# Kernel optimization log

Hardware: AMD Instinct MI355X
Metric: run time of the kernel (lower is better)

The kernel has to match this reference:

```python
import jax, jax.numpy as jnp
import numpy as np

B, H, W, C = 32, 56, 56, 192
WS, SHIFT, HEADS = 7, 3, 6
HEAD_DIM = C // HEADS
SCALE = 0.17677669529663687  # 1/sqrt(32), passed as qk_scale
HIDDEN = 4 * C
N = WS * WS
EPS = 1e-3


def _rel_index(ws):
    coords = np.stack(np.meshgrid(np.arange(ws), np.arange(ws), indexing='ij')).reshape(2, -1)
    rel = (coords[:, :, None] - coords[:, None, :]).transpose(1, 2, 0)
    rel[:, :, 0] += ws - 1
    rel[:, :, 1] += ws - 1
    rel[:, :, 0] *= 2 * ws - 1
    return rel.sum(-1)  # [N, N] int


def _attn_mask(h, w, ws, ss):
    img = np.zeros((h, w), np.float32)
    cnt = 0
    for hs in (slice(0, -ws), slice(-ws, -ss), slice(-ss, None)):
        for wsl in (slice(0, -ws), slice(-ws, -ss), slice(-ss, None)):
            img[hs, wsl] = cnt
            cnt += 1
    win = img.reshape(h // ws, ws, w // ws, ws).transpose(0, 2, 1, 3).reshape(-1, ws * ws)
    diff = win[:, None, :] - win[:, :, None]
    return np.where(diff != 0, -100.0, 0.0).astype(np.float32)  # [nW, N, N]


REL_IDX = jnp.asarray(_rel_index(WS).reshape(-1))          # [N*N]
ATTN_MASK = jnp.asarray(_attn_mask(H, W, WS, SHIFT))       # [nW, N, N]
NW = ATTN_MASK.shape[0]


def _window_partition(x, ws):
    b, h, w, c = x.shape
    x = x.reshape(b, h // ws, ws, w // ws, ws, c).transpose(0, 1, 3, 2, 4, 5)
    return x.reshape(-1, ws, ws, c)


def _window_reverse(x, ws, h, w):
    c = x.shape[-1]
    x = x.reshape(-1, h // ws, w // ws, ws, ws, c).transpose(0, 1, 3, 2, 4, 5)
    return x.reshape(-1, h, w, c)


def _layer_norm(x, g, b):
    mu = jnp.mean(x, axis=-1, keepdims=True)
    var = jnp.var(x, axis=-1, keepdims=True)
    return (x - mu) * jax.lax.rsqrt(var + EPS) * g + b


def _forward(x, ln1_g, ln1_b, w_qkv, b_qkv, bias_table, w_proj, b_proj,
             ln2_g, ln2_b, w_ffn1, bn1_scale, bn1_shift, w_ffn2, bn2_scale, bn2_shift):
    shortcut = x
    h = _layer_norm(x, ln1_g, ln1_b)
    h = jnp.roll(h, (-SHIFT, -SHIFT), axis=(1, 2))
    xw = _window_partition(h, WS).reshape(-1, N, C)  # [B*nW, N, C]

    qkv = xw @ w_qkv + b_qkv                          # [B*nW, N, 3C]
    qkv = qkv.reshape(-1, N, 3, HEADS, HEAD_DIM).transpose(2, 0, 3, 1, 4)
    q, k, v = qkv[0] * SCALE, qkv[1], qkv[2]          # [B*nW, heads, N, hd]

    attn = jnp.einsum('whnd,whmd->whnm', q, k)        # [B*nW, heads, N, N]
    rel_bias = bias_table[REL_IDX].reshape(N, N, HEADS).transpose(2, 0, 1)
    attn = attn + rel_bias[None]
    attn = attn.reshape(-1, NW, HEADS, N, N) + ATTN_MASK[None, :, None]
    attn = jax.nn.softmax(attn.reshape(-1, HEADS, N, N), axis=-1)

    o = jnp.einsum('whnm,whmd->whnd', attn, v)        # [B*nW, heads, N, hd]
    o = o.transpose(0, 2, 1, 3).reshape(-1, N, C)
    o = o @ w_proj + b_proj

    o = _window_reverse(o.reshape(-1, WS, WS, C), WS, H, W)
    o = jnp.roll(o, (SHIFT, SHIFT), axis=(1, 2))
    x = shortcut + o

    y = _layer_norm(x, ln2_g, ln2_b)
    dn = ('NHWC', 'HWIO', 'NHWC')
    y = jax.lax.conv_general_dilated(y, w_ffn1, (1, 1), 'SAME', dimension_numbers=dn)
    y = y * bn1_scale + bn1_shift
    y = jax.nn.gelu(y, approximate=False)
    y = jax.lax.conv_general_dilated(y, w_ffn2, (1, 1), 'SAME', dimension_numbers=dn)
    y = y * bn2_scale + bn2_shift
    return x + y


def setup_inputs() -> dict:
    key = jax.random.key(0)
    ks = jax.random.split(key, 8)
    s = lambda n: 0.02
    return {
        'x': jax.random.normal(ks[0], (B, H, W, C), jnp.float32),
        'ln1_g': jnp.ones((C,), jnp.float32),
        'ln1_b': jnp.zeros((C,), jnp.float32),
        'w_qkv': jax.random.normal(ks[1], (C, 3 * C), jnp.float32) * (C ** -0.5),
        'b_qkv': jnp.zeros((3 * C,), jnp.float32),
        'bias_table': jax.random.truncated_normal(ks[2], -2.0, 2.0, ((2 * WS - 1) ** 2, HEADS), jnp.float32) * 0.02,
        'w_proj': jax.random.normal(ks[3], (C, C), jnp.float32) * (C ** -0.5),
        'b_proj': jnp.zeros((C,), jnp.float32),
        'ln2_g': jnp.ones((C,), jnp.float32),
        'ln2_b': jnp.zeros((C,), jnp.float32),
        'w_ffn1': jax.random.normal(ks[4], (3, 3, C, HIDDEN), jnp.float32) * ((9 * C) ** -0.5),
        'bn1_scale': jnp.ones((HIDDEN,), jnp.float32),
        'bn1_shift': jnp.zeros((HIDDEN,), jnp.float32),
        'w_ffn2': jax.random.normal(ks[5], (1, 1, HIDDEN, C), jnp.float32) * (HIDDEN ** -0.5),
        'bn2_scale': jnp.ones((C,), jnp.float32),
        'bn2_shift': jnp.zeros((C,), jnp.float32),
    }


def reference(x, ln1_g, ln1_b, w_qkv, b_qkv, bias_table, w_proj, b_proj,
              ln2_g, ln2_b, w_ffn1, bn1_scale, bn1_shift, w_ffn2, bn2_scale, bn2_shift):
    return _forward(x, ln1_g, ln1_b, w_qkv, b_qkv, bias_table, w_proj, b_proj,
                    ln2_g, ln2_b, w_ffn1, bn1_scale, bn1_shift, w_ffn2, bn2_scale, bn2_shift)
```

## Files before the change

kernel.cpp:

```cpp
#include <hip/hip_runtime.h>
#include <hip/hip_bf16.h>
#include <math.h>

#define DEVINL __device__ __forceinline__

typedef __bf16 bf16x8 __attribute__((ext_vector_type(8)));
typedef float  f32x4  __attribute__((ext_vector_type(4)));
typedef unsigned int u32x4 __attribute__((ext_vector_type(4)));

DEVINL float bf2f(unsigned short h){ return __builtin_bit_cast(float, (unsigned)h << 16); }
DEVINL unsigned short f2bf(float f){
  unsigned u = __builtin_bit_cast(unsigned, f);
  u += 0x7fffu + ((u >> 16) & 1u);
  return (unsigned short)(u >> 16);
}

DEVINL void gl16(const unsigned short* g, unsigned short* l){
  __builtin_amdgcn_global_load_lds((const __attribute__((address_space(1))) unsigned int*)g,
                                   (__attribute__((address_space(3))) unsigned int*)l,
                                   16, 0, 0);
}

DEVINL unsigned ldsoff(const void* p){
  return (unsigned)(unsigned long long)(const __attribute__((address_space(3))) char*)p;
}
DEVINL bf16x8 dsr16(const unsigned short* p){
  u32x4 r;
  asm volatile("ds_read_b128 %0, %1" : "=v"(r) : "v"(ldsoff(p)));
  return __builtin_bit_cast(bf16x8, r);
}

#define Bn 32
#define Hn 56
#define Wn 56
#define Cn 192
#define WSz 7
#define SHIFTn 3
#define HEADSn 6
#define HDn 32
#define NWIN 49
#define NPIX (Bn*Hn*Wn)
#define HIDDENn 768
#define KCONV (9*Cn)
#define PADH 58
#define QKSCALE 0.17677669529663687f

DEVINL float wave_sum(float v){
  #pragma unroll
  for (int off=32; off; off>>=1) v += __shfl_xor(v, off, 64);
  return v;
}

__global__ __launch_bounds__(256) void k_ln1(const float* __restrict__ x,
                                             const float* __restrict__ g,
                                             const float* __restrict__ bb,
                                             unsigned short* __restrict__ h)
{
  int row  = blockIdx.x*4 + (threadIdx.x >> 6);
  int lane = threadIdx.x & 63;
  int win = row / NWIN, n = row % NWIN;
  int b = win >> 6, rem = win & 63, wh = rem >> 3, ww = rem & 7;
  int i = n / WSz, j = n % WSz;
  int rr = (wh*WSz + i + SHIFTn) % Hn;
  int cc = (ww*WSz + j + SHIFTn) % Wn;
  const float* xr = x + (size_t)((b*Hn + rr)*Wn + cc)*Cn;
  float v0 = xr[lane], v1 = xr[lane+64], v2 = xr[lane+128];
  float s  = wave_sum(v0+v1+v2);
  float sq = wave_sum(v0*v0+v1*v1+v2*v2);
  float mu = s * (1.0f/Cn);
  float var = sq * (1.0f/Cn) - mu*mu;
  float rs = rsqrtf(var + 1e-3f);
  unsigned short* hr = h + (size_t)row*Cn;
  hr[lane]     = f2bf((v0-mu)*rs*g[lane]     + bb[lane]);
  hr[lane+64]  = f2bf((v1-mu)*rs*g[lane+64]  + bb[lane+64]);
  hr[lane+128] = f2bf((v2-mu)*rs*g[lane+128] + bb[lane+128]);
}

__global__ __launch_bounds__(256) void k_ln2(const float* __restrict__ xmid,
                                             const float* __restrict__ g,
                                             const float* __restrict__ bb,
                                             unsigned short* __restrict__ out)
{
  int p    = blockIdx.x*4 + (threadIdx.x >> 6);
  int lane = threadIdx.x & 63;
  int b = p / (Hn*Wn), rc = p % (Hn*Wn);
  int r = rc / Wn, c = rc % Wn;
  const float* xr = xmid + (size_t)p*Cn;
  float v0 = xr[lane], v1 = xr[lane+64], v2 = xr[lane+128];
  float s  = wave_sum(v0+v1+v2);
  float sq = wave_sum(v0*v0+v1*v1+v2*v2);
  float mu = s * (1.0f/Cn);
  float var = sq * (1.0f/Cn) - mu*mu;
  float rs = rsqrtf(var + 1e-3f);
  unsigned short* orow = out + (size_t)((b*PADH + r + 1)*PADH + (c + 1))*Cn;
  orow[lane]     = f2bf((v0-mu)*rs*g[lane]     + bb[lane]);
  orow[lane+64]  = f2bf((v1-mu)*rs*g[lane+64]  + bb[lane+64]);
  orow[lane+128] = f2bf((v2-mu)*rs*g[lane+128] + bb[lane+128]);
}

__global__ __launch_bounds__(256) void k_transpose(const float* __restrict__ in,
                                                   unsigned short* __restrict__ out,
                                                   int K, int N)
{
  int idx = blockIdx.x*256 + threadIdx.x;
  if (idx < K*N){ int k = idx / N, n = idx - k*N; out[(size_t)n*K + k] = f2bf(in[idx]); }
}

__global__ __launch_bounds__(256) void k_attn(const unsigned short* __restrict__ qkv,
                                              const float* __restrict__ bias_table,
                                              unsigned short* __restrict__ o,
                                              int win_base)
{
  __shared__ float qs[NWIN][HDn], ks[NWIN][HDn], vs[NWIN][HDn], S[NWIN][NWIN+1];
  int head = blockIdx.x, lwin = blockIdx.y;
  int gwin = win_base + lwin;
  int tid = threadIdx.x;
  const unsigned short* base = qkv + (size_t)lwin*NWIN*576 + head*HDn;
  for (int t = tid; t < NWIN*HDn; t += 256){
    int n = t >> 5, d = t & 31;
    const unsigned short* rp = base + (size_t)n*576 + d;
    qs[n][d] = bf2f(rp[0]) * QKSCALE;
    ks[n][d] = bf2f(rp[192]);
    vs[n][d] = bf2f(rp[384]);
  }
  __syncthreads();
  int rem = gwin & 63, wh = rem >> 3, ww = rem & 7;
  for (int t = tid; t < NWIN*NWIN; t += 256){
    int p = t / NWIN, q = t - p*NWIN;
    float acc = 0.f;
    #pragma unroll
    for (int d = 0; d < HDn; ++d) acc += qs[p][d]*ks[q][d];
    int pi = p/7, pj = p%7, qi = q/7, qj = q%7;
    int rel = (pi-qi+6)*13 + (pj-qj+6);
    acc += bias_table[rel*HEADSn + head];
    int pr = wh*7+pi, pc = ww*7+pj, qr = wh*7+qi, qc = ww*7+qj;
    int cp = (pr<49?0:(pr<53?1:2))*3 + (pc<49?0:(pc<53?1:2));
    int cq = (qr<49?0:(qr<53?1:2))*3 + (qc<49?0:(qc<53?1:2));
    if (cp != cq) acc -= 100.0f;
    S[p][q] = acc;
  }
  __syncthreads();
  if (tid < NWIN){
    float m = -1e30f;
    for (int q=0;q<NWIN;++q) m = fmaxf(m, S[tid][q]);
    float sum = 0.f;
    for (int q=0;q<NWIN;++q){ float e = expf(S[tid][q]-m); S[tid][q]=e; sum+=e; }
    float inv = 1.0f/sum;
    for (int q=0;q<NWIN;++q) S[tid][q] *= inv;
  }
  __syncthreads();
  for (int t = tid; t < NWIN*HDn; t += 256){
    int n = t >> 5, d = t & 31;
    float acc = 0.f;
    for (int m=0;m<NWIN;++m) acc += S[n][m]*vs[m][d];
    o[((size_t)gwin*NWIN + n)*Cn + head*HDn + d] = f2bf(acc);
  }
}

template<int AMODE, int EPI, int BMt, int BNt>
__global__ __launch_bounds__(256) void k_gemm(const unsigned short* __restrict__ A,
                                              const unsigned short* __restrict__ Bt,
                                              int K, int a_rbase, int o_rbase,
                                              const float* __restrict__ e0,
                                              const float* __restrict__ e1,
                                              const float* __restrict__ e2,
                                              void* __restrict__ out)
{
  constexpr int WMT = BMt/32, WNT = BNt/32;
  constexpr int NIA = BMt/64, NIB = BNt/64;
  __shared__ __align__(16) unsigned short As[BMt*32];
  __shared__ __align__(16) unsigned short Bs[BNt*32];
  int tid = threadIdx.x;
  int bm = blockIdx.y * BMt, bn = blockIdx.x * BNt;
  int wave = tid >> 6, lane = tid & 63;
  int l15 = lane & 15, quad = lane >> 4;
  int wm = (wave & 1) * (BMt/2), wn = (wave >> 1) * (BNt/2);

  int srow = tid >> 2;
  int kc   = (tid & 3) * 8;

  size_t abase[NIA];
  #pragma unroll
  for (int i=0;i<NIA;++i){
    int lrow = bm + i*64 + srow;
    if (AMODE == 0) abase[i] = (size_t)(a_rbase + lrow) * K + kc;
    else {
      int grow = a_rbase + lrow;
      int b = grow / (Hn*Wn), rc = grow % (Hn*Wn);
      int r = rc / Wn, c = rc - r*Wn;
      abase[i] = (size_t)((b*PADH + r)*PADH + c) * Cn + kc;
    }
  }
  size_t bbase[NIB];
  #pragma unroll
  for (int i=0;i<NIB;++i) bbase[i] = (size_t)(bn + i*64 + srow) * K + kc;

  f32x4 acc[WMT][WNT] = {};

  int nkb = K / 32;
  for (int kb = 0; kb < nkb; ++kb){
    int k0 = kb * 32;
    size_t aoff;
    if (AMODE == 0) aoff = (size_t)k0;
    else {
      int tap = k0 / Cn, ci = k0 - tap*Cn;
      int dh = tap/3, dw = tap - dh*3;
      aoff = (size_t)((dh*PADH + dw)*Cn + ci);
    }
    #pragma unroll
    for (int i=0;i<NIA;++i)
      gl16(A + abase[i] + aoff, &As[i*64*32] + (size_t)tid*8);
    #pragma unroll
    for (int i=0;i<NIB;++i)
      gl16(Bt + bbase[i] + (size_t)k0, &Bs[i*64*32] + (size_t)tid*8);
    __syncthreads();

    bf16x8 af[WMT], bfr[WNT];
    #pragma unroll
    for (int mt=0;mt<WMT;++mt) af[mt]  = *(const bf16x8*)&As[(wm + mt*16 + l15)*32 + quad*8];
    #pragma unroll
    for (int nt=0;nt<WNT;++nt) bfr[nt] = *(const bf16x8*)&Bs[(wn + nt*16 + l15)*32 + quad*8];
    #pragma unroll
    for (int mt=0;mt<WMT;++mt)
      #pragma unroll
      for (int nt=0;nt<WNT;++nt)
        acc[mt][nt] = __builtin_amdgcn_mfma_f32_16x16x32_bf16(af[mt], bfr[nt], acc[mt][nt], 0,0,0);
    __syncthreads();
  }

  #pragma unroll
  for (int mt=0; mt<WMT; ++mt)
  #pragma unroll
  for (int nt=0; nt<WNT; ++nt){
    f32x4 a4 = acc[mt][nt];
    int gcol = bn + wn + nt*16 + l15;
    #pragma unroll
    for (int r=0; r<4; ++r){
      int orow = bm + wm + mt*16 + quad*4 + r;
      float v = a4[r];
      if (EPI == 0){
        v += e0[gcol];
        ((unsigned short*)out)[(size_t)orow*576 + gcol] = f2bf(v);
      } else if (EPI == 1){
        v += e0[gcol];
        int grow = o_rbase + orow;
        int win = grow / NWIN, n = grow - win*NWIN;
        int b = win >> 6, rem2 = win & 63, wh = rem2 >> 3, ww = rem2 & 7;
        int ii = n / WSz, jj = n - ii*WSz;
        int fr = (wh*WSz + ii + SHIFTn) % Hn;
        int fc = (ww*WSz + jj + SHIFTn) % Wn;
        size_t idx = (size_t)((b*Hn + fr)*Wn + fc)*Cn + gcol;
        ((float*)out)[idx] = e2[idx] + v;
      } else if (EPI == 2){
        v = v * e0[gcol] + e1[gcol];
        v = 0.5f * v * (1.0f + erff(v * 0.7071067811865476f));
        ((unsigned short*)out)[(size_t)orow*HIDDENn + gcol] = f2bf(v);
      } else {
        v = v * e0[gcol] + e1[gcol];
        int grow = o_rbase + orow;
        v += e2[(size_t)grow*Cn + gcol];
        ((float*)out)[(size_t)grow*Cn + gcol] = v;
      }
    }
  }
}

__global__ __launch_bounds__(512, 1) void k_gemm8conv(
    const unsigned short* __restrict__ A,
    const unsigned short* __restrict__ Bt,
    int a_rbase,
    const float* __restrict__ e0,
    const float* __restrict__ e1,
    unsigned short* __restrict__ out)
{
  __shared__ __align__(16) unsigned short As[2*256*64];
  __shared__ __align__(16) unsigned short Bs[2*256*64];
  const int tid  = threadIdx.x;
  const int wave = tid >> 6, lane = tid & 63;
  const int l15  = lane & 15, quad = lane >> 4;
  const int wm   = (wave & 1) * 128;
  const int wn   = (wave >> 1) * 64;
  const int bm   = blockIdx.y * 256, bn = blockIdx.x * 256;

  const int srow = tid >> 3;
  const int scs  = (tid & 7) ^ (srow & 7);
  const int ldst = tid * 8;

  size_t abase[4], bbase[4];
  #pragma unroll
  for (int i=0;i<4;++i){
    int grow = a_rbase + bm + i*64 + srow;
    int b = grow / (Hn*Wn), rc = grow % (Hn*Wn);
    int r = rc / Wn, c = rc - r*Wn;
    abase[i] = (size_t)((b*PADH + r)*PADH + c)*Cn + scs*8;
    bbase[i] = (size_t)(bn + i*64 + srow)*KCONV + scs*8;
  }

  const int cx0 = ((quad    ) ^ (l15 & 7)) * 8;
  const int cx1 = ((quad + 4) ^ (l15 & 7)) * 8;

  f32x4 acc[8][4] = {};
  bf16x8 af[4][2], bfr[4][2];

  const int ntot = KCONV/64;

  #pragma unroll
  for (int i=0;i<4;++i) gl16(Bt + bbase[i],      Bs + i*4096 + ldst);
  #pragma unroll
  for (int i=0;i<4;++i) gl16(A  + abase[i],      As + i*4096 + ldst);
  #pragma unroll
  for (int i=0;i<4;++i) gl16(Bt + bbase[i] + 64, Bs + 16384 + i*4096 + ldst);
  #pragma unroll
  for (int i=0;i<4;++i) gl16(A  + abase[i] + 64, As + 16384 + i*4096 + ldst);
  asm volatile("s_waitcnt vmcnt(8)" ::: "memory");
  __builtin_amdgcn_s_barrier();

  for (int t = 0; t < ntot; ++t){
    const unsigned short* Ac = As + (t&1)*16384;
    const unsigned short* Bc = Bs + (t&1)*16384;
    unsigned short* Asn = As + (t&1)*16384;
    unsigned short* Bsn = Bs + (t&1)*16384;
    const bool pf = (t+2 < ntot);
    const int t2 = t + 2;
    const int tap2 = t2/3;
    const int dh2 = tap2/3, dw2 = tap2 - dh2*3, ci2 = (t2 - tap2*3)*64;
    const size_t aoff2 = (size_t)(dh2*PADH + dw2)*Cn + ci2;
    const size_t boff2 = (size_t)t2*64;

    #pragma unroll
    for (int mt=0; mt<4; ++mt){
      const unsigned short* rp = Ac + (wm + mt*16 + l15)*64;
      af[mt][0] = dsr16(rp + cx0);
      af[mt][1] = dsr16(rp + cx1);
    }
    #pragma unroll
    for (int nn=0; nn<4; ++nn){
      const unsigned short* rp = Bc + (wn + nn*16 + l15)*64;
      bfr[nn][0] = dsr16(rp + cx0);
      bfr[nn][1] = dsr16(rp + cx1);
    }
    asm volatile("s_waitcnt lgkmcnt(0)" ::: "memory");
    __builtin_amdgcn_sched_barrier(0);
    __builtin_amdgcn_s_barrier();
    if (pf){ gl16(Bt + bbase[0] + boff2, Bsn + 0*4096 + ldst);
             gl16(Bt + bbase[1] + boff2, Bsn + 1*4096 + ldst); }
    __builtin_amdgcn_s_setprio(1);
    #pragma unroll
    for (int mt=0; mt<4; ++mt)
      #pragma unroll
      for (int nn=0; nn<2; ++nn)
        #pragma unroll
        for (int kk=0; kk<2; ++kk)
          acc[mt][nn] = __builtin_amdgcn_mfma_f32_16x16x32_bf16(af[mt][kk], bfr[nn][kk], acc[mt][nn], 0,0,0);
    __builtin_amdgcn_s_setprio(0);
    __builtin_amdgcn_s_barrier();

    if (pf){ gl16(Bt + bbase[2] + boff2, Bsn + 2*4096 + ldst);
             gl16(Bt + bbase[3] + boff2, Bsn + 3*4096 + ldst); }
    __builtin_amdgcn_s_setprio(1);
    #pragma unroll
    for (int mt=0; mt<4; ++mt)
      #pragma unroll
      for (int nn=2; nn<4; ++nn)
        #pragma unroll
        for (int kk=0; kk<2; ++kk)
          acc[mt][nn] = __builtin_amdgcn_mfma_f32_16x16x32_bf16(af[mt][kk], bfr[nn][kk], acc[mt][nn], 0,0,0);
    __builtin_amdgcn_s_setprio(0);
    __builtin_amdgcn_s_barrier();

    #pragma unroll
    for (int mt=0; mt<4; ++mt){
      const unsigned short* rp = Ac + (wm + 64 + mt*16 + l15)*64;
      af[mt][0] = dsr16(rp + cx0);
      af[mt][1] = dsr16(rp + cx1);
    }
    asm volatile("s_waitcnt lgkmcnt(0)" ::: "memory");
    __builtin_amdgcn_sched_barrier(0);
    __builtin_amdgcn_s_barrier();
    if (pf){ gl16(A + abase[0] + aoff2, Asn + 0*4096 + ldst);
             gl16(A + abase[1] + aoff2, Asn + 1*4096 + ldst); }
    __builtin_amdgcn_s_setprio(1);
    #pragma unroll
    for (int mt=0; mt<4; ++mt)
      #pragma unroll
      for (int nn=0; nn<2; ++nn)
        #pragma unroll
        for (int kk=0; kk<2; ++kk)
          acc[4+mt][nn] = __builtin_amdgcn_mfma_f32_16x16x32_bf16(af[mt][kk], bfr[nn][kk], acc[4+mt][nn], 0,0,0);
    __builtin_amdgcn_s_setprio(0);
    __builtin_amdgcn_s_barrier();

    if (pf){ gl16(A + abase[2] + aoff2, Asn + 2*4096 + ldst);
             gl16(A + abase[3] + aoff2, Asn + 3*4096 + ldst); }
    __builtin_amdgcn_s_setprio(1);
    #pragma unroll
    for (int mt=0; mt<4; ++mt)
      #pragma unroll
      for (int nn=2; nn<4; ++nn)
        #pragma unroll
        for (int kk=0; kk<2; ++kk)
          acc[4+mt][nn] = __builtin_amdgcn_mfma_f32_16x16x32_bf16(af[mt][kk], bfr[nn][kk], acc[4+mt][nn], 0,0,0);
    __builtin_amdgcn_s_setprio(0);
    if (pf)                  { asm volatile("s_waitcnt vmcnt(8)" ::: "memory"); }
    else if (t+1 < ntot)     { asm volatile("s_waitcnt vmcnt(0)" ::: "memory"); }
    __builtin_amdgcn_s_barrier();
  }

  const int orow0 = bm + wm + quad*4;
  #pragma unroll
  for (int nn=0; nn<4; ++nn){
    int gcol = bn + wn + nn*16 + l15;
    float s0 = e0[gcol], s1 = e1[gcol];
    #pragma unroll
    for (int mt=0; mt<8; ++mt){
      #pragma unroll
      for (int r=0; r<4; ++r){
        float v = acc[mt][nn][r] * s0 + s1;
        v = 0.5f * v * (1.0f + erff(v * 0.7071067811865476f));
        out[(size_t)(orow0 + mt*16 + r)*HIDDENn + gcol] = f2bf(v);
      }
    }
  }
}

extern "C" void kernel_launch(void* const* d_in, const int* in_sizes, int n_in,
                              void* d_out, int out_size, void* d_ws, size_t ws_size,
                              hipStream_t stream)
{
  const float* x        = (const float*)d_in[0];
  const float* ln1_g    = (const float*)d_in[1];
  const float* ln1_b    = (const float*)d_in[2];
  const float* w_qkv    = (const float*)d_in[3];
  const float* b_qkv    = (const float*)d_in[4];
  const float* btab     = (const float*)d_in[5];
  const float* w_proj   = (const float*)d_in[6];
  const float* b_proj   = (const float*)d_in[7];
  const float* ln2_g    = (const float*)d_in[8];
  const float* ln2_b    = (const float*)d_in[9];
  const float* w_ffn1   = (const float*)d_in[10];
  const float* bn1_s    = (const float*)d_in[11];
  const float* bn1_sh   = (const float*)d_in[12];
  const float* w_ffn2   = (const float*)d_in[13];
  const float* bn2_s    = (const float*)d_in[14];
  const float* bn2_sh   = (const float*)d_in[15];

  const size_t szA   = 41337344;
  const size_t xmsz  = (size_t)NPIX*Cn*4;
  const size_t wtsz  = 221184 + 73728 + 2654208 + 294912;
  int nch = 8;
  for (int cand = 1; cand <= 8; cand <<= 1){
    size_t need = szA + ((size_t)NPIX*HIDDENn*2)/cand + xmsz + wtsz + (1u<<20);
    if (need <= ws_size){ nch = cand; break; }
  }
  const int mc = NPIX / nch;
  const int wc = 2048 / nch;

  char* ws = (char*)d_ws;
  size_t off = 0;
  unsigned short* h      = (unsigned short*)(ws + off);
  unsigned short* ln2pad = (unsigned short*)(ws + off);  off += szA;
  unsigned short* qc     = (unsigned short*)(ws + off);
  unsigned short* hc     = (unsigned short*)(ws + off);  off += ((size_t)NPIX*HIDDENn*2)/nch;
  float*          xmid   = (float*)(ws + off);           off += xmsz;
  unsigned short* wTq    = (unsigned short*)(ws + off);  off += 221184;
  unsigned short* wTp    = (unsigned short*)(ws + off);  off += 73728;
  unsigned short* wTf1   = (unsigned short*)(ws + off);  off += 2654208;
  unsigned short* wTf2   = (unsigned short*)(ws + off);
  float*          outp   = (float*)d_out;
  unsigned short* obuf   = (unsigned short*)d_out;

  dim3 blk(256);

  k_transpose<<<(192*576 + 255)/256,  blk, 0, stream>>>(w_qkv,  wTq,  192, 576);
  k_transpose<<<(192*192 + 255)/256,  blk, 0, stream>>>(w_proj, wTp,  192, 192);
  k_transpose<<<(1728*768 + 255)/256, blk, 0, stream>>>(w_ffn1, wTf1, 1728, 768);
  k_transpose<<<(768*192 + 255)/256,  blk, 0, stream>>>(w_ffn2, wTf2, 768, 192);

  k_ln1<<<NPIX/4, blk, 0, stream>>>(x, ln1_g, ln1_b, h);

  for (int c = 0; c < nch; ++c){
    int rbase = c * mc;
    k_gemm<0,0,128,64><<<dim3(576/64, mc/128), blk, 0, stream>>>(
        h, wTq, 192, rbase, 0, b_qkv, nullptr, nullptr, qc);
    k_attn<<<dim3(HEADSn, wc), blk, 0, stream>>>(qc, btab, obuf, c*wc);
  }

  k_gemm<0,1,128,64><<<dim3(192/64, NPIX/128), blk, 0, stream>>>(
      obuf, wTp, 192, 0, 0, b_proj, nullptr, x, xmid);

  hipMemsetAsync(ln2pad, 0, (size_t)Bn*PADH*PADH*Cn*2, stream);
  k_ln2<<<NPIX/4, blk, 0, stream>>>(xmid, ln2_g, ln2_b, ln2pad);

  for (int c = 0; c < nch; ++c){
    int rbase = c * mc;
    k_gemm8conv<<<dim3(HIDDENn/256, mc/256), dim3(512), 0, stream>>>(
        ln2pad, wTf1, rbase, bn1_s, bn1_sh, hc);
    k_gemm<0,3,128,64><<<dim3(192/64, mc/128), blk, 0, stream>>>(
        hc, wTf2, 768, 0, rbase, bn2_s, bn2_sh, xmid, outp);
  }
}
```

Measured before the change: 1.062 ms.

## Restructure conv GEMM pipeline to prefetch next stage with fewer barriers, add XCD swizzle

The conv-as-GEMM kernel's double-buffered pipeline now prefetches only one tile ahead into the opposite buffer, instead of two ahead into the current buffer. Each iteration issues the loads before the LDS-read wait and drops two of the four barriers, using finer vmcnt waits so A rows are ready before they are read. Workgroup indices are also remapped so that consecutive tiles land on the same XCD, which is meant to improve L2 reuse of the shared weight and input tiles. The shorter prefetch distance may expose more global-load latency, and the tighter waitcnt logic carries a correctness risk if the counts are off.

```diff
diff --git a/kernel.cpp b/kernel.cpp
--- a/kernel.cpp
+++ b/kernel.cpp
@@ -280,7 +280,14 @@
   const int l15  = lane & 15, quad = lane >> 4;
   const int wm   = (wave & 1) * 128;
   const int wn   = (wave >> 1) * 64;
-  const int bm   = blockIdx.y * 256, bn = blockIdx.x * 256;
+
+  const int nwg = gridDim.x * gridDim.y;
+  const int lin = blockIdx.y * gridDim.x + blockIdx.x;
+  const int q8 = nwg >> 3, r8 = nwg & 7;
+  const int xcd = lin & 7, cidx = lin >> 3;
+  const int swz = (xcd < r8 ? xcd*(q8+1) : r8*(q8+1) + (xcd - r8)*q8) + cidx;
+  const int bn = (swz % gridDim.x) * 256;
+  const int bm = (swz / gridDim.x) * 256;
 
   const int srow = tid >> 3;
   const int scs  = (tid & 7) ^ (srow & 7);
@@ -304,28 +311,28 @@
 
   const int ntot = KCONV/64;
 
-  #pragma unroll
-  for (int i=0;i<4;++i) gl16(Bt + bbase[i],      Bs + i*4096 + ldst);
-  #pragma unroll
-  for (int i=0;i<4;++i) gl16(A  + abase[i],      As + i*4096 + ldst);
-  #pragma unroll
-  for (int i=0;i<4;++i) gl16(Bt + bbase[i] + 64, Bs + 16384 + i*4096 + ldst);
-  #pragma unroll
-  for (int i=0;i<4;++i) gl16(A  + abase[i] + 64, As + 16384 + i*4096 + ldst);
-  asm volatile("s_waitcnt vmcnt(8)" ::: "memory");
+  gl16(Bt + bbase[0], Bs + 0*4096 + ldst);
+  gl16(Bt + bbase[1], Bs + 1*4096 + ldst);
+  gl16(Bt + bbase[2], Bs + 2*4096 + ldst);
+  gl16(Bt + bbase[3], Bs + 3*4096 + ldst);
+  gl16(A  + abase[0], As + 0*4096 + ldst);
+  gl16(A  + abase[2], As + 2*4096 + ldst);
+  gl16(A  + abase[1], As + 1*4096 + ldst);
+  gl16(A  + abase[3], As + 3*4096 + ldst);
+  asm volatile("s_waitcnt vmcnt(2)" ::: "memory");
   __builtin_amdgcn_s_barrier();
 
   for (int t = 0; t < ntot; ++t){
     const unsigned short* Ac = As + (t&1)*16384;
     const unsigned short* Bc = Bs + (t&1)*16384;
-    unsigned short* Asn = As + (t&1)*16384;
-    unsigned short* Bsn = Bs + (t&1)*16384;
-    const bool pf = (t+2 < ntot);
-    const int t2 = t + 2;
-    const int tap2 = t2/3;
-    const int dh2 = tap2/3, dw2 = tap2 - dh2*3, ci2 = (t2 - tap2*3)*64;
-    const size_t aoff2 = (size_t)(dh2*PADH + dw2)*Cn + ci2;
-    const size_t boff2 = (size_t)t2*64;
+    unsigned short* Asn = As + ((t&1)^1)*16384;
+    unsigned short* Bsn = Bs + ((t&1)^1)*16384;
+    const bool pf = (t+1 < ntot);
+    const int t1 = t + 1;
+    const int tap1 = t1/3;
+    const int dh1 = tap1/3, dw1 = tap1 - dh1*3, ci1 = (t1 - tap1*3)*64;
+    const size_t aoff1 = (size_t)(dh1*PADH + dw1)*Cn + ci1;
+    const size_t boff1 = (size_t)t1*64;
 
     #pragma unroll
     for (int mt=0; mt<4; ++mt){
@@ -339,11 +346,10 @@
       bfr[nn][0] = dsr16(rp + cx0);
       bfr[nn][1] = dsr16(rp + cx1);
     }
+    if (pf){ gl16(Bt + bbase[0] + boff1, Bsn + 0*4096 + ldst);
+             gl16(Bt + bbase[1] + boff1, Bsn + 1*4096 + ldst); }
     asm volatile("s_waitcnt lgkmcnt(0)" ::: "memory");
     __builtin_amdgcn_sched_barrier(0);
-    __builtin_amdgcn_s_barrier();
-    if (pf){ gl16(Bt + bbase[0] + boff2, Bsn + 0*4096 + ldst);
-             gl16(Bt + bbase[1] + boff2, Bsn + 1*4096 + ldst); }
     __builtin_amdgcn_s_setprio(1);
     #pragma unroll
     for (int mt=0; mt<4; ++mt)
@@ -353,10 +359,9 @@
         for (int kk=0; kk<2; ++kk)
           acc[mt][nn] = __builtin_amdgcn_mfma_f32_16x16x32_bf16(af[mt][kk], bfr[nn][kk], acc[mt][nn], 0,0,0);
     __builtin_amdgcn_s_setprio(0);
-    __builtin_amdgcn_s_barrier();
-
-    if (pf){ gl16(Bt + bbase[2] + boff2, Bsn + 2*4096 + ldst);
-             gl16(Bt + bbase[3] + boff2, Bsn + 3*4096 + ldst); }
+
+    if (pf){ gl16(Bt + bbase[2] + boff1, Bsn + 2*4096 + ldst);
+             gl16(Bt + bbase[3] + boff1, Bsn + 3*4096 + ldst); }
     __builtin_amdgcn_s_setprio(1);
     #pragma unroll
     for (int mt=0; mt<4; ++mt)
@@ -366,6 +371,8 @@
         for (int kk=0; kk<2; ++kk)
           acc[mt][nn] = __builtin_amdgcn_mfma_f32_16x16x32_bf16(af[mt][kk], bfr[nn][kk], acc[mt][nn], 0,0,0);
     __builtin_amdgcn_s_setprio(0);
+    if (pf) { asm volatile("s_waitcnt vmcnt(4)" ::: "memory"); }
+    else    { asm volatile("s_waitcnt vmcnt(0)" ::: "memory"); }
     __builtin_amdgcn_s_barrier();
 
     #pragma unroll
@@ -374,11 +381,10 @@
       af[mt][0] = dsr16(rp + cx0);
       af[mt][1] = dsr16(rp + cx1);
     }
+    if (pf){ gl16(A + abase[0] + aoff1, Asn + 0*4096 + ldst);
+             gl16(A + abase[2] + aoff1, Asn + 2*4096 + ldst); }
     asm volatile("s_waitcnt lgkmcnt(0)" ::: "memory");
     __builtin_amdgcn_sched_barrier(0);
-    __builtin_amdgcn_s_barrier();
-    if (pf){ gl16(A + abase[0] + aoff2, Asn + 0*4096 + ldst);
-             gl16(A + abase[1] + aoff2, Asn + 1*4096 + ldst); }
     __builtin_amdgcn_s_setprio(1);
     #pragma unroll
     for (int mt=0; mt<4; ++mt)
@@ -388,10 +394,9 @@
         for (int kk=0; kk<2; ++kk)
           acc[4+mt][nn] = __builtin_amdgcn_mfma_f32_16x16x32_bf16(af[mt][kk], bfr[nn][kk], acc[4+mt][nn], 0,0,0);
     __builtin_amdgcn_s_setprio(0);
-    __builtin_amdgcn_s_barrier();
-
-    if (pf){ gl16(A + abase[2] + aoff2, Asn + 2*4096 + ldst);
-             gl16(A + abase[3] + aoff2, Asn + 3*4096 + ldst); }
+
+    if (pf){ gl16(A + abase[1] + aoff1, Asn + 1*4096 + ldst);
+             gl16(A + abase[3] + aoff1, Asn + 3*4096 + ldst); }
     __builtin_amdgcn_s_setprio(1);
     #pragma unroll
     for (int mt=0; mt<4; ++mt)
@@ -401,8 +406,7 @@
         for (int kk=0; kk<2; ++kk)
           acc[4+mt][nn] = __builtin_amdgcn_mfma_f32_16x16x32_bf16(af[mt][kk], bfr[nn][kk], acc[4+mt][nn], 0,0,0);
     __builtin_amdgcn_s_setprio(0);
-    if (pf)                  { asm volatile("s_waitcnt vmcnt(8)" ::: "memory"); }
-    else if (t+1 < ntot)     { asm volatile("s_waitcnt vmcnt(0)" ::: "memory"); }
+    if (pf) { asm volatile("s_waitcnt vmcnt(2)" ::: "memory"); }
     __builtin_amdgcn_s_barrier();
   }
 
```

New measurement: 1.128 ms. +6.2%, slower.

## Swizzle conv GEMM blocks across XCDs and re-plan workspace to cut FFN chunking

Applied to the files above, without the earlier changes.

Remaps the conv-GEMM workgroup index so that consecutive tiles land on the same XCD, improving L2 reuse of A and B tiles on the chiplet layout. The workspace is reorganised: xmid now lives in the output buffer, and obuf moves into the workspace next to a fixed 8-chunk qkv buffer. This frees space so the FFN stage can run in fewer, larger chunks and with fewer launches. The risk is aliasing: xmid and the output share memory, and the final GEMM reads xmid while writing outp, which is only safe if each element is read before it is written.

```diff
diff --git a/kernel.cpp b/kernel.cpp
--- a/kernel.cpp
+++ b/kernel.cpp
@@ -280,7 +280,14 @@
   const int l15  = lane & 15, quad = lane >> 4;
   const int wm   = (wave & 1) * 128;
   const int wn   = (wave >> 1) * 64;
-  const int bm   = blockIdx.y * 256, bn = blockIdx.x * 256;
+
+  const int nwg = gridDim.x * gridDim.y;
+  const int lin = blockIdx.y * gridDim.x + blockIdx.x;
+  const int q8 = nwg >> 3, r8 = nwg & 7;
+  const int xcd = lin & 7, cidx = lin >> 3;
+  const int swz = (xcd < r8 ? xcd*(q8+1) : r8*(q8+1) + (xcd - r8)*q8) + cidx;
+  const int bn = (swz % gridDim.x) * 256;
+  const int bm = (swz / gridDim.x) * 256;
 
   const int srow = tid >> 3;
   const int scs  = (tid & 7) ^ (srow & 7);
@@ -445,29 +452,35 @@
   const float* bn2_sh   = (const float*)d_in[15];
 
   const size_t szA   = 41337344;
-  const size_t xmsz  = (size_t)NPIX*Cn*4;
+  const int    nq    = 8;
+  const size_t qc_sz = (size_t)NPIX*576*2/nq;
+  const size_t ob_sz = (size_t)NPIX*Cn*2;
   const size_t wtsz  = 221184 + 73728 + 2654208 + 294912;
-  int nch = 8;
+  int nf = 8;
   for (int cand = 1; cand <= 8; cand <<= 1){
-    size_t need = szA + ((size_t)NPIX*HIDDENn*2)/cand + xmsz + wtsz + (1u<<20);
-    if (need <= ws_size){ nch = cand; break; }
-  }
-  const int mc = NPIX / nch;
-  const int wc = 2048 / nch;
+    size_t bsz_c = (size_t)NPIX*HIDDENn*2/cand;
+    if (bsz_c < qc_sz + ob_sz) bsz_c = qc_sz + ob_sz;
+    if (szA + bsz_c + wtsz + (1u<<20) <= ws_size){ nf = cand; break; }
+  }
+  size_t bsz = (size_t)NPIX*HIDDENn*2/nf;
+  if (bsz < qc_sz + ob_sz) bsz = qc_sz + ob_sz;
+  const int mc_q = NPIX / nq;
+  const int wc_q = 2048 / nq;
+  const int mc_f = NPIX / nf;
 
   char* ws = (char*)d_ws;
-  size_t off = 0;
-  unsigned short* h      = (unsigned short*)(ws + off);
-  unsigned short* ln2pad = (unsigned short*)(ws + off);  off += szA;
-  unsigned short* qc     = (unsigned short*)(ws + off);
-  unsigned short* hc     = (unsigned short*)(ws + off);  off += ((size_t)NPIX*HIDDENn*2)/nch;
-  float*          xmid   = (float*)(ws + off);           off += xmsz;
+  unsigned short* h      = (unsigned short*)ws;
+  unsigned short* ln2pad = (unsigned short*)ws;
+  unsigned short* qc     = (unsigned short*)(ws + szA);
+  unsigned short* obuf   = (unsigned short*)(ws + szA + qc_sz);
+  unsigned short* hc     = (unsigned short*)(ws + szA);
+  size_t off = szA + bsz;
   unsigned short* wTq    = (unsigned short*)(ws + off);  off += 221184;
   unsigned short* wTp    = (unsigned short*)(ws + off);  off += 73728;
   unsigned short* wTf1   = (unsigned short*)(ws + off);  off += 2654208;
   unsigned short* wTf2   = (unsigned short*)(ws + off);
+  float*          xmid   = (float*)d_out;
   float*          outp   = (float*)d_out;
-  unsigned short* obuf   = (unsigned short*)d_out;
 
   dim3 blk(256);
 
@@ -478,11 +491,11 @@
 
   k_ln1<<<NPIX/4, blk, 0, stream>>>(x, ln1_g, ln1_b, h);
 
-  for (int c = 0; c < nch; ++c){
-    int rbase = c * mc;
-    k_gemm<0,0,128,64><<<dim3(576/64, mc/128), blk, 0, stream>>>(
+  for (int c = 0; c < nq; ++c){
+    int rbase = c * mc_q;
+    k_gemm<0,0,128,64><<<dim3(576/64, mc_q/128), blk, 0, stream>>>(
         h, wTq, 192, rbase, 0, b_qkv, nullptr, nullptr, qc);
-    k_attn<<<dim3(HEADSn, wc), blk, 0, stream>>>(qc, btab, obuf, c*wc);
+    k_attn<<<dim3(HEADSn, wc_q), blk, 0, stream>>>(qc, btab, obuf, c*wc_q);
   }
 
   k_gemm<0,1,128,64><<<dim3(192/64, NPIX/128), blk, 0, stream>>>(
@@ -491,11 +504,11 @@
   hipMemsetAsync(ln2pad, 0, (size_t)Bn*PADH*PADH*Cn*2, stream);
   k_ln2<<<NPIX/4, blk, 0, stream>>>(xmid, ln2_g, ln2_b, ln2pad);
 
-  for (int c = 0; c < nch; ++c){
-    int rbase = c * mc;
-    k_gemm8conv<<<dim3(HIDDENn/256, mc/256), dim3(512), 0, stream>>>(
+  for (int c = 0; c < nf; ++c){
+    int rbase = c * mc_f;
+    k_gemm8conv<<<dim3(HIDDENn/256, mc_f/256), dim3(512), 0, stream>>>(
         ln2pad, wTf1, rbase, bn1_s, bn1_sh, hc);
-    k_gemm<0,3,128,64><<<dim3(192/64, mc/128), blk, 0, stream>>>(
+    k_gemm<0,3,128,64><<<dim3(192/64, mc_f/128), blk, 0, stream>>>(
         hc, wTf2, 768, 0, rbase, bn2_s, bn2_sh, xmid, outp);
   }
 }
```

Result: slower. 1.145 ms (+7.8%).

## Restructure conv GEMM barriers, add XCD-aware block swizzle, reshuffle workspace buffers

Applied to the files above, without the earlier changes.

The 3x3-conv FFN GEMM now issues each operand's prefetch in one batch of four loads instead of two pairs. This removes two of the four block barriers per K-step, and a partial lgkmcnt wait lets MFMAs start before all LDS reads finish. Workgroups are remapped so consecutive tiles land on the same XCD, aiming for better L2 reuse. The workspace layout also changes: xmid now lives in the output buffer and obuf moves into the workspace, which may allow fewer chunks. The cost is reduced load/compute interleaving and possible aliasing hazards between xmid and the final output.

```diff
diff --git a/kernel.cpp b/kernel.cpp
--- a/kernel.cpp
+++ b/kernel.cpp
@@ -280,7 +280,14 @@
   const int l15  = lane & 15, quad = lane >> 4;
   const int wm   = (wave & 1) * 128;
   const int wn   = (wave >> 1) * 64;
-  const int bm   = blockIdx.y * 256, bn = blockIdx.x * 256;
+
+  const int nwg = gridDim.x * gridDim.y;
+  const int lin = blockIdx.y * gridDim.x + blockIdx.x;
+  const int q8 = nwg >> 3, r8 = nwg & 7;
+  const int xcd = lin & 7, cidx = lin >> 3;
+  const int swz = (xcd < r8 ? xcd*(q8+1) : r8*(q8+1) + (xcd - r8)*q8) + cidx;
+  const int bn = (swz % gridDim.x) * 256;
+  const int bm = (swz / gridDim.x) * 256;
 
   const int srow = tid >> 3;
   const int scs  = (tid & 7) ^ (srow & 7);
@@ -339,11 +346,8 @@
       bfr[nn][0] = dsr16(rp + cx0);
       bfr[nn][1] = dsr16(rp + cx1);
     }
-    asm volatile("s_waitcnt lgkmcnt(0)" ::: "memory");
+    asm volatile("s_waitcnt lgkmcnt(4)" ::: "memory");
     __builtin_amdgcn_sched_barrier(0);
-    __builtin_amdgcn_s_barrier();
-    if (pf){ gl16(Bt + bbase[0] + boff2, Bsn + 0*4096 + ldst);
-             gl16(Bt + bbase[1] + boff2, Bsn + 1*4096 + ldst); }
     __builtin_amdgcn_s_setprio(1);
     #pragma unroll
     for (int mt=0; mt<4; ++mt)
@@ -353,10 +357,8 @@
         for (int kk=0; kk<2; ++kk)
           acc[mt][nn] = __builtin_amdgcn_mfma_f32_16x16x32_bf16(af[mt][kk], bfr[nn][kk], acc[mt][nn], 0,0,0);
     __builtin_amdgcn_s_setprio(0);
-    __builtin_amdgcn_s_barrier();
-
-    if (pf){ gl16(Bt + bbase[2] + boff2, Bsn + 2*4096 + ldst);
-             gl16(Bt + bbase[3] + boff2, Bsn + 3*4096 + ldst); }
+    asm volatile("s_waitcnt lgkmcnt(0)" ::: "memory");
+    __builtin_amdgcn_sched_barrier(0);
     __builtin_amdgcn_s_setprio(1);
     #pragma unroll
     for (int mt=0; mt<4; ++mt)
@@ -367,6 +369,10 @@
           acc[mt][nn] = __builtin_amdgcn_mfma_f32_16x16x32_bf16(af[mt][kk], bfr[nn][kk], acc[mt][nn], 0,0,0);
     __builtin_amdgcn_s_setprio(0);
     __builtin_amdgcn_s_barrier();
+    if (pf){ gl16(Bt + bbase[0] + boff2, Bsn + 0*4096 + ldst);
+             gl16(Bt + bbase[1] + boff2, Bsn + 1*4096 + ldst);
+             gl16(Bt + bbase[2] + boff2, Bsn + 2*4096 + ldst);
+             gl16(Bt + bbase[3] + boff2, Bsn + 3*4096 + ldst); }
 
     #pragma unroll
     for (int mt=0; mt<4; ++mt){
@@ -376,31 +382,20 @@
     }
     asm volatile("s_waitcnt lgkmcnt(0)" ::: "memory");
     __builtin_amdgcn_sched_barrier(0);
-    __builtin_amdgcn_s_barrier();
-    if (pf){ gl16(A + abase[0] + aoff2, Asn + 0*4096 + ldst);
-             gl16(A + abase[1] + aoff2, Asn + 1*4096 + ldst); }
     __builtin_amdgcn_s_setprio(1);
     #pragma unroll
     for (int mt=0; mt<4; ++mt)
       #pragma unroll
-      for (int nn=0; nn<2; ++nn)
+      for (int nn=0; nn<4; ++nn)
         #pragma unroll
         for (int kk=0; kk<2; ++kk)
           acc[4+mt][nn] = __builtin_amdgcn_mfma_f32_16x16x32_bf16(af[mt][kk], bfr[nn][kk], acc[4+mt][nn], 0,0,0);
     __builtin_amdgcn_s_setprio(0);
     __builtin_amdgcn_s_barrier();
-
-    if (pf){ gl16(A + abase[2] + aoff2, Asn + 2*4096 + ldst);
+    if (pf){ gl16(A + abase[0] + aoff2, Asn + 0*4096 + ldst);
+             gl16(A + abase[1] + aoff2, Asn + 1*4096 + ldst);
+             gl16(A + abase[2] + aoff2, Asn + 2*4096 + ldst);
              gl16(A + abase[3] + aoff2, Asn + 3*4096 + ldst); }
-    __builtin_amdgcn_s_setprio(1);
-    #pragma unroll
-    for (int mt=0; mt<4; ++mt)
-      #pragma unroll
-      for (int nn=2; nn<4; ++nn)
-        #pragma unroll
-        for (int kk=0; kk<2; ++kk)
-          acc[4+mt][nn] = __builtin_amdgcn_mfma_f32_16x16x32_bf16(af[mt][kk], bfr[nn][kk], acc[4+mt][nn], 0,0,0);
-    __builtin_amdgcn_s_setprio(0);
     if (pf)                  { asm volatile("s_waitcnt vmcnt(8)" ::: "memory"); }
     else if (t+1 < ntot)     { asm volatile("s_waitcnt vmcnt(0)" ::: "memory"); }
     __builtin_amdgcn_s_barrier();
@@ -445,29 +440,35 @@
   const float* bn2_sh   = (const float*)d_in[15];
 
   const size_t szA   = 41337344;
-  const size_t xmsz  = (size_t)NPIX*Cn*4;
+  const size_t ob_sz = (size_t)NPIX*Cn*2;
   const size_t wtsz  = 221184 + 73728 + 2654208 + 294912;
   int nch = 8;
   for (int cand = 1; cand <= 8; cand <<= 1){
-    size_t need = szA + ((size_t)NPIX*HIDDENn*2)/cand + xmsz + wtsz + (1u<<20);
-    if (need <= ws_size){ nch = cand; break; }
-  }
+    size_t qcsz  = (size_t)NPIX*1152/cand;
+    size_t hcsz  = (size_t)NPIX*1536/cand;
+    size_t bsz_c = qcsz + ob_sz;
+    if (hcsz > bsz_c) bsz_c = hcsz;
+    if (szA + bsz_c + wtsz + (1u<<20) <= ws_size){ nch = cand; break; }
+  }
+  const size_t qc_sz = (size_t)NPIX*1152/nch;
+  size_t bsz = qc_sz + ob_sz;
+  { size_t hcsz = (size_t)NPIX*1536/nch; if (hcsz > bsz) bsz = hcsz; }
   const int mc = NPIX / nch;
   const int wc = 2048 / nch;
 
   char* ws = (char*)d_ws;
-  size_t off = 0;
-  unsigned short* h      = (unsigned short*)(ws + off);
-  unsigned short* ln2pad = (unsigned short*)(ws + off);  off += szA;
-  unsigned short* qc     = (unsigned short*)(ws + off);
-  unsigned short* hc     = (unsigned short*)(ws + off);  off += ((size_t)NPIX*HIDDENn*2)/nch;
-  float*          xmid   = (float*)(ws + off);           off += xmsz;
+  unsigned short* h      = (unsigned short*)ws;
+  unsigned short* ln2pad = (unsigned short*)ws;
+  unsigned short* qc     = (unsigned short*)(ws + szA);
+  unsigned short* obuf   = (unsigned short*)(ws + szA + qc_sz);
+  unsigned short* hc     = (unsigned short*)(ws + szA);
+  size_t off = szA + bsz;
   unsigned short* wTq    = (unsigned short*)(ws + off);  off += 221184;
   unsigned short* wTp    = (unsigned short*)(ws + off);  off += 73728;
   unsigned short* wTf1   = (unsigned short*)(ws + off);  off += 2654208;
   unsigned short* wTf2   = (unsigned short*)(ws + off);
+  float*          xmid   = (float*)d_out;
   float*          outp   = (float*)d_out;
-  unsigned short* obuf   = (unsigned short*)d_out;
 
   dim3 blk(256);
 
```

Measured after the change: 1.049 ms. No clear change (-1.2%).
